# Optimization experiments

Measured on AMD Instinct MI355X. Metric: run time of the kernel, lower is better.

## Reference

```python
import jax, jax.numpy as jnp
import numpy as np

N_EMBD = 1024
N_HEAD = 16
HEAD_DIM = N_EMBD // N_HEAD


def setup_inputs() -> dict:
    key = jax.random.key(0)
    kx, kqkv, kw, kb = jax.random.split(key, 4)
    B, T = 4, 2048
    x = jax.random.normal(kx, (B, T, N_EMBD), dtype=jnp.float32)
    # nn.Linear weights stored [out, in]; apply as x @ W.T
    w_qkv = jax.random.normal(kqkv, (3 * N_EMBD, N_EMBD), dtype=jnp.float32) * (N_EMBD ** -0.5)
    w_out = jax.random.normal(kw, (N_EMBD, N_EMBD), dtype=jnp.float32) * (N_EMBD ** -0.5)
    b_out = jax.random.normal(kb, (N_EMBD,), dtype=jnp.float32) * 0.01
    return {"x": x, "w_qkv": w_qkv, "w_out": w_out, "b_out": b_out}


def reference(x, w_qkv, w_out, b_out):
    B, T, C = x.shape
    H, D = N_HEAD, HEAD_DIM
    qkv = jnp.einsum('btc,fc->btf', x, w_qkv)  # [B,T,3C]
    q, k, v = jnp.split(qkv, 3, axis=-1)
    q = q.reshape(B, T, H, D).transpose(0, 2, 1, 3)  # [B,H,T,D]
    k = k.reshape(B, T, H, D).transpose(0, 2, 1, 3)
    v = v.reshape(B, T, H, D).transpose(0, 2, 1, 3)
    att = jnp.einsum('bhqd,bhkd->bhqk', q, k) * (D ** -0.5)  # [B,H,T,T]
    causal = jnp.tril(jnp.ones((T, T), dtype=bool))
    att = jnp.where(causal[None, None], att, jnp.float32(-jnp.inf))
    att = jax.nn.softmax(att, axis=-1)
    out = jnp.einsum('bhqk,bhkd->bhqd', att, v)  # [B,H,T,D]
    out = out.transpose(0, 2, 1, 3).reshape(B, T, C)
    return jnp.einsum('btc,oc->bto', out, w_out) + b_out
```

## Files before the change

### kernel.cpp

```cpp
#include <hip/hip_runtime.h>
#include <stdint.h>

#define SEQ 2048
#define C3 3072
#define C1 1024

typedef __bf16 bf16x8 __attribute__((ext_vector_type(8)));
typedef short short8 __attribute__((ext_vector_type(8)));
typedef float f32x4 __attribute__((ext_vector_type(4)));
typedef float f32x16 __attribute__((ext_vector_type(16)));
typedef unsigned uintx2 __attribute__((ext_vector_type(2)));
typedef const __attribute__((address_space(1))) void gv_t;
typedef __attribute__((address_space(3))) void lv_t;

#if __has_builtin(__builtin_amdgcn_exp2f)
#define EXP2(x) __builtin_amdgcn_exp2f(x)
#else
#define EXP2(x) exp2f(x)
#endif

static __device__ __forceinline__ unsigned short f2bf(float f) {
  union { float ff; unsigned u; } x; x.ff = f;
  unsigned u = x.u + 0x7FFFu + ((x.u >> 16) & 1u);
  return (unsigned short)(u >> 16);
}
static __device__ __forceinline__ unsigned rne2(float lo, float hi) {
  return (unsigned)f2bf(lo) | ((unsigned)f2bf(hi) << 16);
}
static __device__ __forceinline__ unsigned pk2(float lo, float hi) {
  union { float f; unsigned u; } a, b; a.f = lo; b.f = hi;
  return __builtin_amdgcn_perm(b.u, a.u, 0x07060302);
}

static __device__ __forceinline__ void plswap(unsigned a, unsigned b,
                                              unsigned& o0, unsigned& o1) {
#if __has_builtin(__builtin_amdgcn_permlane32_swap)
  uintx2 r = __builtin_amdgcn_permlane32_swap(a, b, false, false);
  o0 = r[0]; o1 = r[1];
#else
  asm volatile("v_permlane32_swap_b32 %0, %1" : "+v"(a), "+v"(b));
  o0 = a; o1 = b;
#endif
}

__global__ void k_cvt3(const float* __restrict__ ia, const float* __restrict__ ib,
                       const float* __restrict__ ic, unsigned short* __restrict__ oa,
                       unsigned short* __restrict__ ob, unsigned short* __restrict__ oc) {
  int blk = blockIdx.x;
  const float* in; unsigned short* out; int base;
  if (blk < 8192)      { in = ia; out = oa; base = blk; }
  else if (blk < 11264){ in = ib; out = ob; base = blk - 8192; }
  else                 { in = ic; out = oc; base = blk - 11264; }
  int i = base * 256 + threadIdx.x;
  f32x4 v = ((const f32x4*)in)[i];
  ushort4 o;
  o.x = f2bf(v[0]); o.y = f2bf(v[1]); o.z = f2bf(v[2]); o.w = f2bf(v[3]);
  ((ushort4*)out)[i] = o;
}

template<int MODE>
__global__ __launch_bounds__(256, 3) void k_gemm(
    const unsigned short* __restrict__ A, const unsigned short* __restrict__ B,
    void* __restrict__ Cout, const float* __restrict__ bias,
    unsigned short* __restrict__ vTout, int M, int N, int K)
{
  __shared__ unsigned short As[128 * 64];
  __shared__ unsigned short Bs[128 * 64];
  const int tid = threadIdx.x;
  const int w = tid >> 6, l = tid & 63;
  const int lane15 = l & 15, quad = l >> 4;
  const int m0 = blockIdx.y * 128, n0 = blockIdx.x * 128;
  const int wm = (w >> 1) * 64, wn = (w & 1) * 64;

  f32x4 acc[4][4];
#pragma unroll
  for (int i = 0; i < 4; i++)
#pragma unroll
    for (int j = 0; j < 4; j++) acc[i][j] = (f32x4){0.f, 0.f, 0.f, 0.f};

  const int srow = l >> 3;
  const int g_off = ((l & 7) ^ (srow & 7)) * 8;
  const unsigned short* Ab = A + (size_t)(m0 + w * 32 + srow) * K + g_off;
  const unsigned short* Bb = B + (size_t)(n0 + w * 32 + srow) * K + g_off;
  const int rsl = lane15 & 7;

  for (int k0 = 0; k0 < K; k0 += 64) {
    __syncthreads();
#pragma unroll
    for (int i = 0; i < 4; i++) {
      int rb = w * 32 + i * 8;
      __builtin_amdgcn_global_load_lds((gv_t*)(Ab + (size_t)(i * 8) * K + k0),
                                       (lv_t*)&As[rb * 64], 16, 0, 0);
      __builtin_amdgcn_global_load_lds((gv_t*)(Bb + (size_t)(i * 8) * K + k0),
                                       (lv_t*)&Bs[rb * 64], 16, 0, 0);
    }
    __syncthreads();
#pragma unroll
    for (int s = 0; s < 2; s++) {
      bf16x8 af[4], bfr[4];
      const int slot = ((s * 4 + quad) ^ rsl) * 8;
#pragma unroll
      for (int t = 0; t < 4; t++) {
        af[t]  = *(const bf16x8*)&As[(wm + t * 16 + lane15) * 64 + slot];
        bfr[t] = *(const bf16x8*)&Bs[(wn + t * 16 + lane15) * 64 + slot];
      }
#pragma unroll
      for (int i = 0; i < 4; i++)
#pragma unroll
        for (int j = 0; j < 4; j++)
          acc[i][j] = __builtin_amdgcn_mfma_f32_16x16x32_bf16(af[i], bfr[j], acc[i][j], 0, 0, 0);
    }
  }

  if (MODE == 0) {
    if (n0 >= 2048) {
#pragma unroll
      for (int i = 0; i < 4; i++) {
        int rowb = m0 + wm + i * 16 + quad * 4;
        int bb = rowb >> 11, t = rowb & 2047;
#pragma unroll
        for (int j = 0; j < 4; j++) {
          int hd = n0 + wn + j * 16 + lane15 - 2048;
          unsigned short* vp = vTout +
              ((size_t)((bb << 4) + (hd >> 6)) * 64 + (hd & 63)) * SEQ + t;
          *(uint2*)vp = make_uint2(rne2(acc[i][j][0], acc[i][j][1]),
                                   rne2(acc[i][j][2], acc[i][j][3]));
        }
      }
    } else {
      unsigned short* Cp = (unsigned short*)Cout;
      const float s = (n0 < 1024) ? 0.18033688f : 1.0f;
#pragma unroll
      for (int i = 0; i < 4; i++) {
        int rowb = m0 + wm + i * 16 + quad * 4;
#pragma unroll
        for (int j = 0; j < 4; j++) {
          int col = n0 + wn + j * 16 + lane15;
#pragma unroll
          for (int r = 0; r < 4; r++)
            Cp[(size_t)(rowb + r) * N + col] = f2bf(acc[i][j][r] * s);
        }
      }
    }
  } else {
    float* Cp = (float*)Cout;
#pragma unroll
    for (int i = 0; i < 4; i++) {
      int rowb = m0 + wm + i * 16 + quad * 4;
#pragma unroll
      for (int j = 0; j < 4; j++) {
        int col = n0 + wn + j * 16 + lane15;
        float bv = bias[col];
#pragma unroll
        for (int r = 0; r < 4; r++)
          Cp[(size_t)(rowb + r) * N + col] = acc[i][j][r] + bv;
      }
    }
  }
}


static __device__ __forceinline__ void stage_kv(
    unsigned short* bufp, const unsigned short* __restrict__ qkv,
    const unsigned short* __restrict__ vT, size_t tokb, int bh, int h,
    int k0, int w, int krow_l, int kslot, int vrow_l, int vslot)
{
  unsigned short* Kb = bufp;
  unsigned short* Vb = bufp + 8192;
#pragma unroll
  for (int i = 0; i < 4; i++) {
    int rb = (w * 4 + i) * 8;
    int row = rb + krow_l;
    int ck = kslot ^ (row & 7);
    const unsigned short* g = qkv + (tokb + k0 + row) * C3 + C1 + h * 64 + ck * 8;
    __builtin_amdgcn_global_load_lds((gv_t*)g, (lv_t*)&Kb[rb * 64], 16, 0, 0);
  }
#pragma unroll
  for (int i = 0; i < 4; i++) {
    int rb = (w * 4 + i) * 4;
    int row = rb + vrow_l;
    int ck = vslot ^ (row & 15);
    const unsigned short* g = vT + ((size_t)bh * 64 + row) * SEQ + k0 + ck * 8;
    __builtin_amdgcn_global_load_lds((gv_t*)g, (lv_t*)&Vb[rb * 128], 16, 0, 0);
  }
}

static __device__ __forceinline__ void attn_tile(
    f32x16* O, float& lrun, const bf16x8* qf,
    const unsigned short* Kb, const unsigned short* Vb,
    bool diag, int k0, int qmy, int w, int l31, int hl)
{
#pragma unroll
  for (int ht = 0; ht < 2; ht++) {
    if (diag && (ht * 2 > w)) continue;
    const bool two = !diag || (ht * 2 + 1 <= w);

#pragma unroll
    for (int lm = 0; lm < 2; lm++) {
      if (lm == 1 && !two) continue;
      const int mt = ht * 2 + lm;

      f32x16 stL;
#pragma unroll
      for (int i = 0; i < 16; i++) stL[i] = -16.f;
      {
        int row = mt * 32 + l31;
        const unsigned short* kr = &Kb[row * 64];
        __builtin_amdgcn_s_setprio(1);
#pragma unroll
        for (int ks = 0; ks < 4; ks++) {
          bf16x8 a = *(const bf16x8*)&kr[((((ks << 1) | hl)) ^ (row & 7)) * 8];
          stL = __builtin_amdgcn_mfma_f32_32x32x16_bf16(a, qf[ks], stL, 0, 0, 0);
        }
        __builtin_amdgcn_s_setprio(0);
      }

      if (diag && mt == w) {
#pragma unroll
        for (int r = 0; r < 16; r++) {
          int key = k0 + w * 32 + (r & 3) + ((r >> 2) << 3) + (hl << 2);
          if (key > qmy) stL[r] = -1e30f;
        }
      }

      float ps0 = 0.f, ps1 = 0.f, ps2 = 0.f, ps3 = 0.f;
      unsigned pk[8];
#pragma unroll
      for (int r = 0; r < 16; r += 4) {
        float p0 = EXP2(stL[r]);
        float p1 = EXP2(stL[r + 1]);
        float p2 = EXP2(stL[r + 2]);
        float p3 = EXP2(stL[r + 3]);
        ps0 += p0; ps1 += p1; ps2 += p2; ps3 += p3;
        pk[(r >> 1)]     = pk2(p0, p1);
        pk[(r >> 1) + 1] = pk2(p2, p3);
      }
      lrun += (ps0 + ps1) + (ps2 + ps3);

      bf16x8 vf[2][2];
#pragma unroll
      for (int e = 0; e < 2; e++) {
        int kk = ht * 4 + lm * 2 + e;
#pragma unroll
        for (int dt = 0; dt < 2; dt++) {
          int row = dt * 32 + l31;
          vf[e][dt] = *(const bf16x8*)&Vb[row * 128 + (((2 * kk + hl)) ^ (row & 15)) * 8];
        }
      }

#pragma unroll
      for (int e = 0; e < 2; e++) {
        union { unsigned u[4]; bf16x8 v; } Bf;
        plswap(pk[4 * e],     pk[4 * e + 2], Bf.u[0], Bf.u[2]);
        plswap(pk[4 * e + 1], pk[4 * e + 3], Bf.u[1], Bf.u[3]);
        __builtin_amdgcn_s_setprio(1);
        O[0] = __builtin_amdgcn_mfma_f32_32x32x16_bf16(vf[e][0], Bf.v, O[0], 0, 0, 0);
        O[1] = __builtin_amdgcn_mfma_f32_32x32x16_bf16(vf[e][1], Bf.v, O[1], 0, 0, 0);
        __builtin_amdgcn_s_setprio(0);
      }
    }
  }
}

static __device__ __forceinline__ void attn_epi(
    const f32x16* O, float lrun, unsigned short* buf,
    unsigned short* __restrict__ att, size_t tokb, int q0, int h,
    int w, int l, int l31, int hl)
{
  lrun += __shfl_xor(lrun, 32, 64);
  float linv = __builtin_amdgcn_rcpf(lrun);
  unsigned* epi32 = (unsigned*)buf;
  const int base = w * 2304 + l31 * 72;
  __builtin_amdgcn_s_waitcnt(0);
#pragma unroll
  for (int dt = 0; dt < 2; dt++)
#pragma unroll
    for (int c = 0; c < 4; c++) {
      int d0 = dt * 32 + c * 8 + hl * 4;
      epi32[(base + d0) >> 1]     = rne2(O[dt][4 * c] * linv, O[dt][4 * c + 1] * linv);
      epi32[(base + d0 + 2) >> 1] = rne2(O[dt][4 * c + 2] * linv, O[dt][4 * c + 3] * linv);
    }
  __builtin_amdgcn_s_waitcnt(0);
  {
    int q = l >> 1, hf = l & 1;
    const unsigned short* ep = &buf[w * 2304 + q * 72 + hf * 32];
    unsigned short* og = att + (tokb + q0 + w * 32 + q) * C1 + h * 64 + hf * 32;
#pragma unroll
    for (int c2 = 0; c2 < 4; c2++)
      *(bf16x8*)(og + c2 * 8) = *(const bf16x8*)&ep[c2 * 8];
  }
}

__global__ __launch_bounds__(256, 2) void k_attn(
    const unsigned short* __restrict__ qkv, const unsigned short* __restrict__ vT,
    unsigned short* __restrict__ att)
{
  __shared__ unsigned short buf[2][16384];
  const int tid = threadIdx.x;
  const int w = tid >> 6, l = tid & 63;
  const int l31 = l & 31, hl = l >> 5;
  const int bh = blockIdx.x, b = bh >> 4, h = bh & 15;
  const int yq = blockIdx.y;
  const int qt_lo = yq, qt_hi = 15 - yq;
  const int q0l = qt_lo << 7, q0h = qt_hi << 7;
  const int nkt = qt_hi + 1;
  const size_t tokb = (size_t)b * SEQ;
  const int qmy_l = q0l + w * 32 + l31;
  const int qmy_h = q0h + w * 32 + l31;

  const int krow_l = l >> 3, kslot = l & 7;
  const int vrow_l = l >> 4, vslot = l & 15;

  bf16x8 qfh[4], qfl[4];
  {
    const unsigned short* qph = qkv + (tokb + q0h + w * 32 + l31) * C3 + h * 64 + hl * 8;
    const unsigned short* qpl = qkv + (tokb + q0l + w * 32 + l31) * C3 + h * 64 + hl * 8;
#pragma unroll
    for (int ks = 0; ks < 4; ks++) {
      qfh[ks] = *(const bf16x8*)(qph + ks * 16);
      qfl[ks] = *(const bf16x8*)(qpl + ks * 16);
    }
  }

  f32x16 Oh[2], Ol[2];
#pragma unroll
  for (int i = 0; i < 16; i++) { Oh[0][i] = 0.f; Oh[1][i] = 0.f; Ol[0][i] = 0.f; Ol[1][i] = 0.f; }
  float lrh = 0.f, lrl = 0.f;

  stage_kv(&buf[0][0], qkv, vT, tokb, bh, h, 0, w, krow_l, kslot, vrow_l, vslot);

  int cur = 0;
  for (int kt = 0; kt < nkt; kt++) {
    asm volatile("s_waitcnt vmcnt(0)" ::: "memory");
    __builtin_amdgcn_s_barrier();
    if (kt + 1 < nkt)
      stage_kv(&buf[cur ^ 1][0], qkv, vT, tokb, bh, h, (kt + 1) << 7,
               w, krow_l, kslot, vrow_l, vslot);

    const unsigned short* Kb = &buf[cur][0];
    const unsigned short* Vb = &buf[cur][8192];
    const int k0 = kt << 7;

    attn_tile(Oh, lrh, qfh, Kb, Vb, kt == qt_hi, k0, qmy_h, w, l31, hl);
    if (kt <= qt_lo)
      attn_tile(Ol, lrl, qfl, Kb, Vb, kt == qt_lo, k0, qmy_l, w, l31, hl);

    cur ^= 1;
  }

  __syncthreads();
  attn_epi(Oh, lrh, &buf[0][0], att, tokb, q0h, h, w, l, l31, hl);
  attn_epi(Ol, lrl, &buf[0][0], att, tokb, q0l, h, w, l, l31, hl);
}

extern "C" void kernel_launch(void* const* d_in, const int* in_sizes, int n_in,
                              void* d_out, int out_size, void* d_ws, size_t ws_size,
                              hipStream_t stream) {
  const float* x     = (const float*)d_in[0];
  const float* w_qkv = (const float*)d_in[1];
  const float* w_out = (const float*)d_in[2];
  const float* b_out = (const float*)d_in[3];
  float* out = (float*)d_out;

  unsigned short* xb  = (unsigned short*)d_ws;
  unsigned short* wqb = xb  + (size_t)8192 * 1024;
  unsigned short* wob = wqb + (size_t)3072 * 1024;
  unsigned short* qkv = wob + (size_t)1024 * 1024;
  unsigned short* att = qkv + (size_t)8192 * 3072;
  unsigned short* vT  = att + (size_t)8192 * 1024;

  k_cvt3<<<12288, 256, 0, stream>>>(x, w_qkv, w_out, xb, wqb, wob);
  k_gemm<0><<<dim3(24, 64), 256, 0, stream>>>(xb, wqb, (void*)qkv, nullptr, vT, 8192, 3072, 1024);
  k_attn<<<dim3(64, 8), 256, 0, stream>>>(qkv, vT, att);
  k_gemm<1><<<dim3(8, 64), 256, 0, stream>>>(att, wob, (void*)out, b_out, nullptr, 8192, 1024, 1024);
}
```

Before: 221.8 us.

## Read V fragments directly from global memory and stage only K in LDS

```diff
diff --git a/kernel.cpp b/kernel.cpp
--- a/kernel.cpp
+++ b/kernel.cpp
@@ -160,13 +160,10 @@
 }
 
 
-static __device__ __forceinline__ void stage_kv(
-    unsigned short* bufp, const unsigned short* __restrict__ qkv,
-    const unsigned short* __restrict__ vT, size_t tokb, int bh, int h,
-    int k0, int w, int krow_l, int kslot, int vrow_l, int vslot)
-{
-  unsigned short* Kb = bufp;
-  unsigned short* Vb = bufp + 8192;
+static __device__ __forceinline__ void stage_k(
+    unsigned short* Kb, const unsigned short* __restrict__ qkv,
+    size_t tokb, int h, int k0, int w, int krow_l, int kslot)
+{
 #pragma unroll
   for (int i = 0; i < 4; i++) {
     int rb = (w * 4 + i) * 8;
@@ -175,19 +172,11 @@
     const unsigned short* g = qkv + (tokb + k0 + row) * C3 + C1 + h * 64 + ck * 8;
     __builtin_amdgcn_global_load_lds((gv_t*)g, (lv_t*)&Kb[rb * 64], 16, 0, 0);
   }
-#pragma unroll
-  for (int i = 0; i < 4; i++) {
-    int rb = (w * 4 + i) * 4;
-    int row = rb + vrow_l;
-    int ck = vslot ^ (row & 15);
-    const unsigned short* g = vT + ((size_t)bh * 64 + row) * SEQ + k0 + ck * 8;
-    __builtin_amdgcn_global_load_lds((gv_t*)g, (lv_t*)&Vb[rb * 128], 16, 0, 0);
-  }
 }
 
 static __device__ __forceinline__ void attn_tile(
     f32x16* O, float& lrun, const bf16x8* qf,
-    const unsigned short* Kb, const unsigned short* Vb,
+    const unsigned short* Kb, const unsigned short* __restrict__ vTb,
     bool diag, int k0, int qmy, int w, int l31, int hl)
 {
 #pragma unroll
@@ -213,6 +202,17 @@
           stL = __builtin_amdgcn_mfma_f32_32x32x16_bf16(a, qf[ks], stL, 0, 0, 0);
         }
         __builtin_amdgcn_s_setprio(0);
+      }
+
+      bf16x8 vf[2][2];
+#pragma unroll
+      for (int e = 0; e < 2; e++) {
+        int kk = ht * 4 + lm * 2 + e;
+#pragma unroll
+        for (int dt = 0; dt < 2; dt++) {
+          int row = dt * 32 + l31;
+          vf[e][dt] = *(const bf16x8*)&vTb[(size_t)row * SEQ + k0 + (2 * kk + hl) * 8];
+        }
       }
 
       if (diag && mt == w) {
@@ -237,17 +237,6 @@
       }
       lrun += (ps0 + ps1) + (ps2 + ps3);
 
-      bf16x8 vf[2][2];
-#pragma unroll
-      for (int e = 0; e < 2; e++) {
-        int kk = ht * 4 + lm * 2 + e;
-#pragma unroll
-        for (int dt = 0; dt < 2; dt++) {
-          int row = dt * 32 + l31;
-          vf[e][dt] = *(const bf16x8*)&Vb[row * 128 + (((2 * kk + hl)) ^ (row & 15)) * 8];
-        }
-      }
-
 #pragma unroll
       for (int e = 0; e < 2; e++) {
         union { unsigned u[4]; bf16x8 v; } Bf;
@@ -291,11 +280,11 @@
   }
 }
 
-__global__ __launch_bounds__(256, 2) void k_attn(
+__global__ __launch_bounds__(256, 3) void k_attn(
     const unsigned short* __restrict__ qkv, const unsigned short* __restrict__ vT,
     unsigned short* __restrict__ att)
 {
-  __shared__ unsigned short buf[2][16384];
+  __shared__ unsigned short buf[2][8192];
   const int tid = threadIdx.x;
   const int w = tid >> 6, l = tid & 63;
   const int l31 = l & 31, hl = l >> 5;
@@ -309,7 +298,7 @@
   const int qmy_h = q0h + w * 32 + l31;
 
   const int krow_l = l >> 3, kslot = l & 7;
-  const int vrow_l = l >> 4, vslot = l & 15;
+  const unsigned short* vTb = vT + (size_t)bh * 64 * SEQ;
 
   bf16x8 qfh[4], qfl[4];
   {
@@ -327,23 +316,21 @@
   for (int i = 0; i < 16; i++) { Oh[0][i] = 0.f; Oh[1][i] = 0.f; Ol[0][i] = 0.f; Ol[1][i] = 0.f; }
   float lrh = 0.f, lrl = 0.f;
 
-  stage_kv(&buf[0][0], qkv, vT, tokb, bh, h, 0, w, krow_l, kslot, vrow_l, vslot);
+  stage_k(&buf[0][0], qkv, tokb, h, 0, w, krow_l, kslot);
 
   int cur = 0;
   for (int kt = 0; kt < nkt; kt++) {
     asm volatile("s_waitcnt vmcnt(0)" ::: "memory");
     __builtin_amdgcn_s_barrier();
     if (kt + 1 < nkt)
-      stage_kv(&buf[cur ^ 1][0], qkv, vT, tokb, bh, h, (kt + 1) << 7,
-               w, krow_l, kslot, vrow_l, vslot);
+      stage_k(&buf[cur ^ 1][0], qkv, tokb, h, (kt + 1) << 7, w, krow_l, kslot);
 
     const unsigned short* Kb = &buf[cur][0];
-    const unsigned short* Vb = &buf[cur][8192];
     const int k0 = kt << 7;
 
-    attn_tile(Oh, lrh, qfh, Kb, Vb, kt == qt_hi, k0, qmy_h, w, l31, hl);
+    attn_tile(Oh, lrh, qfh, Kb, vTb, kt == qt_hi, k0, qmy_h, w, l31, hl);
     if (kt <= qt_lo)
-      attn_tile(Ol, lrl, qfl, Kb, Vb, kt == qt_lo, k0, qmy_l, w, l31, hl);
+      attn_tile(Ol, lrl, qfl, Kb, vTb, kt == qt_lo, k0, qmy_l, w, l31, hl);
 
     cur ^= 1;
   }
```

New measurement: 287.1 us. 1.29x slower.

## Single-buffer V in attention to fit three blocks per CU; coarsen convert kernel

Applied to the files above, without the earlier changes.

```diff
diff --git a/kernel.cpp b/kernel.cpp
--- a/kernel.cpp
+++ b/kernel.cpp
@@ -48,14 +48,18 @@
                        unsigned short* __restrict__ ob, unsigned short* __restrict__ oc) {
   int blk = blockIdx.x;
   const float* in; unsigned short* out; int base;
-  if (blk < 8192)      { in = ia; out = oa; base = blk; }
-  else if (blk < 11264){ in = ib; out = ob; base = blk - 8192; }
-  else                 { in = ic; out = oc; base = blk - 11264; }
-  int i = base * 256 + threadIdx.x;
-  f32x4 v = ((const f32x4*)in)[i];
-  ushort4 o;
-  o.x = f2bf(v[0]); o.y = f2bf(v[1]); o.z = f2bf(v[2]); o.w = f2bf(v[3]);
-  ((ushort4*)out)[i] = o;
+  if (blk < 2048)     { in = ia; out = oa; base = blk; }
+  else if (blk < 2816){ in = ib; out = ob; base = blk - 2048; }
+  else                { in = ic; out = oc; base = blk - 2816; }
+  int i0 = base * 1024 + threadIdx.x;
+#pragma unroll
+  for (int j = 0; j < 4; j++) {
+    int i = i0 + j * 256;
+    f32x4 v = ((const f32x4*)in)[i];
+    ushort4 o;
+    o.x = f2bf(v[0]); o.y = f2bf(v[1]); o.z = f2bf(v[2]); o.w = f2bf(v[3]);
+    ((ushort4*)out)[i] = o;
+  }
 }
 
 template<int MODE>
@@ -160,13 +164,10 @@
 }
 
 
-static __device__ __forceinline__ void stage_kv(
-    unsigned short* bufp, const unsigned short* __restrict__ qkv,
-    const unsigned short* __restrict__ vT, size_t tokb, int bh, int h,
-    int k0, int w, int krow_l, int kslot, int vrow_l, int vslot)
-{
-  unsigned short* Kb = bufp;
-  unsigned short* Vb = bufp + 8192;
+static __device__ __forceinline__ void stage_k(
+    unsigned short* Kb, const unsigned short* __restrict__ qkv,
+    size_t tokb, int h, int k0, int w, int krow_l, int kslot)
+{
 #pragma unroll
   for (int i = 0; i < 4; i++) {
     int rb = (w * 4 + i) * 8;
@@ -175,6 +176,12 @@
     const unsigned short* g = qkv + (tokb + k0 + row) * C3 + C1 + h * 64 + ck * 8;
     __builtin_amdgcn_global_load_lds((gv_t*)g, (lv_t*)&Kb[rb * 64], 16, 0, 0);
   }
+}
+
+static __device__ __forceinline__ void stage_v(
+    unsigned short* Vb, const unsigned short* __restrict__ vT,
+    int bh, int k0, int w, int vrow_l, int vslot)
+{
 #pragma unroll
   for (int i = 0; i < 4; i++) {
     int rb = (w * 4 + i) * 4;
@@ -291,11 +298,12 @@
   }
 }
 
-__global__ __launch_bounds__(256, 2) void k_attn(
+__global__ __launch_bounds__(256, 3) void k_attn(
     const unsigned short* __restrict__ qkv, const unsigned short* __restrict__ vT,
     unsigned short* __restrict__ att)
 {
-  __shared__ unsigned short buf[2][16384];
+  __shared__ unsigned short bufK[2][8192];
+  __shared__ unsigned short bufV[8192];
   const int tid = threadIdx.x;
   const int w = tid >> 6, l = tid & 63;
   const int l31 = l & 31, hl = l >> 5;
@@ -327,30 +335,33 @@
   for (int i = 0; i < 16; i++) { Oh[0][i] = 0.f; Oh[1][i] = 0.f; Ol[0][i] = 0.f; Ol[1][i] = 0.f; }
   float lrh = 0.f, lrl = 0.f;
 
-  stage_kv(&buf[0][0], qkv, vT, tokb, bh, h, 0, w, krow_l, kslot, vrow_l, vslot);
+  stage_k(&bufK[0][0], qkv, tokb, h, 0, w, krow_l, kslot);
+  stage_v(&bufV[0], vT, bh, 0, w, vrow_l, vslot);
 
   int cur = 0;
   for (int kt = 0; kt < nkt; kt++) {
     asm volatile("s_waitcnt vmcnt(0)" ::: "memory");
     __builtin_amdgcn_s_barrier();
     if (kt + 1 < nkt)
-      stage_kv(&buf[cur ^ 1][0], qkv, vT, tokb, bh, h, (kt + 1) << 7,
-               w, krow_l, kslot, vrow_l, vslot);
-
-    const unsigned short* Kb = &buf[cur][0];
-    const unsigned short* Vb = &buf[cur][8192];
+      stage_k(&bufK[cur ^ 1][0], qkv, tokb, h, (kt + 1) << 7, w, krow_l, kslot);
+
+    const unsigned short* Kb = &bufK[cur][0];
     const int k0 = kt << 7;
 
-    attn_tile(Oh, lrh, qfh, Kb, Vb, kt == qt_hi, k0, qmy_h, w, l31, hl);
+    attn_tile(Oh, lrh, qfh, Kb, bufV, kt == qt_hi, k0, qmy_h, w, l31, hl);
     if (kt <= qt_lo)
-      attn_tile(Ol, lrl, qfl, Kb, Vb, kt == qt_lo, k0, qmy_l, w, l31, hl);
+      attn_tile(Ol, lrl, qfl, Kb, bufV, kt == qt_lo, k0, qmy_l, w, l31, hl);
+
+    __builtin_amdgcn_s_barrier();
+    if (kt + 1 < nkt)
+      stage_v(&bufV[0], vT, bh, (kt + 1) << 7, w, vrow_l, vslot);
 
     cur ^= 1;
   }
 
   __syncthreads();
-  attn_epi(Oh, lrh, &buf[0][0], att, tokb, q0h, h, w, l, l31, hl);
-  attn_epi(Ol, lrl, &buf[0][0], att, tokb, q0l, h, w, l, l31, hl);
+  attn_epi(Oh, lrh, &bufK[0][0], att, tokb, q0h, h, w, l, l31, hl);
+  attn_epi(Ol, lrl, &bufK[0][0], att, tokb, q0l, h, w, l, l31, hl);
 }
 
 extern "C" void kernel_launch(void* const* d_in, const int* in_sizes, int n_in,
@@ -369,7 +380,7 @@
   unsigned short* att = qkv + (size_t)8192 * 3072;
   unsigned short* vT  = att + (size_t)8192 * 1024;
 
-  k_cvt3<<<12288, 256, 0, stream>>>(x, w_qkv, w_out, xb, wqb, wob);
+  k_cvt3<<<3072, 256, 0, stream>>>(x, w_qkv, w_out, xb, wqb, wob);
   k_gemm<0><<<dim3(24, 64), 256, 0, stream>>>(xb, wqb, (void*)qkv, nullptr, vT, 8192, 3072, 1024);
   k_attn<<<dim3(64, 8), 256, 0, stream>>>(qkv, vT, att);
   k_gemm<1><<<dim3(8, 64), 256, 0, stream>>>(att, wob, (void*)out, b_out, nullptr, 8192, 1024, 1024);
```

Result: slower. 257.5 us (+16.1%).

## Split hi/lo query tiles across eight waves in attention; widen cast kernel work

Applied to the files above, without the earlier changes.

```diff
diff --git a/kernel.cpp b/kernel.cpp
--- a/kernel.cpp
+++ b/kernel.cpp
@@ -48,14 +48,18 @@
                        unsigned short* __restrict__ ob, unsigned short* __restrict__ oc) {
   int blk = blockIdx.x;
   const float* in; unsigned short* out; int base;
-  if (blk < 8192)      { in = ia; out = oa; base = blk; }
-  else if (blk < 11264){ in = ib; out = ob; base = blk - 8192; }
-  else                 { in = ic; out = oc; base = blk - 11264; }
-  int i = base * 256 + threadIdx.x;
-  f32x4 v = ((const f32x4*)in)[i];
-  ushort4 o;
-  o.x = f2bf(v[0]); o.y = f2bf(v[1]); o.z = f2bf(v[2]); o.w = f2bf(v[3]);
-  ((ushort4*)out)[i] = o;
+  if (blk < 2048)     { in = ia; out = oa; base = blk; }
+  else if (blk < 2816){ in = ib; out = ob; base = blk - 2048; }
+  else                { in = ic; out = oc; base = blk - 2816; }
+  int i0 = base * 1024 + threadIdx.x;
+#pragma unroll
+  for (int j = 0; j < 4; j++) {
+    int i = i0 + j * 256;
+    f32x4 v = ((const f32x4*)in)[i];
+    ushort4 o;
+    o.x = f2bf(v[0]); o.y = f2bf(v[1]); o.z = f2bf(v[2]); o.w = f2bf(v[3]);
+    ((ushort4*)out)[i] = o;
+  }
 }
 
 template<int MODE>
@@ -163,21 +167,23 @@
 static __device__ __forceinline__ void stage_kv(
     unsigned short* bufp, const unsigned short* __restrict__ qkv,
     const unsigned short* __restrict__ vT, size_t tokb, int bh, int h,
-    int k0, int w, int krow_l, int kslot, int vrow_l, int vslot)
+    int k0, int w, int l)
 {
   unsigned short* Kb = bufp;
   unsigned short* Vb = bufp + 8192;
-#pragma unroll
-  for (int i = 0; i < 4; i++) {
-    int rb = (w * 4 + i) * 8;
+  const int krow_l = l >> 3, kslot = l & 7;
+  const int vrow_l = l >> 4, vslot = l & 15;
+#pragma unroll
+  for (int i = 0; i < 2; i++) {
+    int rb = (w * 2 + i) * 8;
     int row = rb + krow_l;
     int ck = kslot ^ (row & 7);
     const unsigned short* g = qkv + (tokb + k0 + row) * C3 + C1 + h * 64 + ck * 8;
     __builtin_amdgcn_global_load_lds((gv_t*)g, (lv_t*)&Kb[rb * 64], 16, 0, 0);
   }
 #pragma unroll
-  for (int i = 0; i < 4; i++) {
-    int rb = (w * 4 + i) * 4;
+  for (int i = 0; i < 2; i++) {
+    int rb = (w * 2 + i) * 4;
     int row = rb + vrow_l;
     int ck = vslot ^ (row & 15);
     const unsigned short* g = vT + ((size_t)bh * 64 + row) * SEQ + k0 + ck * 8;
@@ -188,12 +194,12 @@
 static __device__ __forceinline__ void attn_tile(
     f32x16* O, float& lrun, const bf16x8* qf,
     const unsigned short* Kb, const unsigned short* Vb,
-    bool diag, int k0, int qmy, int w, int l31, int hl)
+    bool diag, int k0, int qmy, int w4, int l31, int hl)
 {
 #pragma unroll
   for (int ht = 0; ht < 2; ht++) {
-    if (diag && (ht * 2 > w)) continue;
-    const bool two = !diag || (ht * 2 + 1 <= w);
+    if (diag && (ht * 2 > w4)) continue;
+    const bool two = !diag || (ht * 2 + 1 <= w4);
 
 #pragma unroll
     for (int lm = 0; lm < 2; lm++) {
@@ -215,10 +221,10 @@
         __builtin_amdgcn_s_setprio(0);
       }
 
-      if (diag && mt == w) {
+      if (diag && mt == w4) {
 #pragma unroll
         for (int r = 0; r < 16; r++) {
-          int key = k0 + w * 32 + (r & 3) + ((r >> 2) << 3) + (hl << 2);
+          int key = k0 + w4 * 32 + (r & 3) + ((r >> 2) << 3) + (hl << 2);
           if (key > qmy) stL[r] = -1e30f;
         }
       }
@@ -264,14 +270,13 @@
 
 static __device__ __forceinline__ void attn_epi(
     const f32x16* O, float lrun, unsigned short* buf,
-    unsigned short* __restrict__ att, size_t tokb, int q0, int h,
+    unsigned short* __restrict__ att, size_t tokb, int qwbase, int h,
     int w, int l, int l31, int hl)
 {
   lrun += __shfl_xor(lrun, 32, 64);
   float linv = __builtin_amdgcn_rcpf(lrun);
   unsigned* epi32 = (unsigned*)buf;
   const int base = w * 2304 + l31 * 72;
-  __builtin_amdgcn_s_waitcnt(0);
 #pragma unroll
   for (int dt = 0; dt < 2; dt++)
 #pragma unroll
@@ -284,73 +289,63 @@
   {
     int q = l >> 1, hf = l & 1;
     const unsigned short* ep = &buf[w * 2304 + q * 72 + hf * 32];
-    unsigned short* og = att + (tokb + q0 + w * 32 + q) * C1 + h * 64 + hf * 32;
+    unsigned short* og = att + (tokb + qwbase + q) * C1 + h * 64 + hf * 32;
 #pragma unroll
     for (int c2 = 0; c2 < 4; c2++)
       *(bf16x8*)(og + c2 * 8) = *(const bf16x8*)&ep[c2 * 8];
   }
 }
 
-__global__ __launch_bounds__(256, 2) void k_attn(
+__global__ __launch_bounds__(512, 2) void k_attn(
     const unsigned short* __restrict__ qkv, const unsigned short* __restrict__ vT,
     unsigned short* __restrict__ att)
 {
   __shared__ unsigned short buf[2][16384];
   const int tid = threadIdx.x;
   const int w = tid >> 6, l = tid & 63;
+  const int w4 = w & 3;
+  const bool hi = (w < 4);
   const int l31 = l & 31, hl = l >> 5;
   const int bh = blockIdx.x, b = bh >> 4, h = bh & 15;
   const int yq = blockIdx.y;
   const int qt_lo = yq, qt_hi = 15 - yq;
-  const int q0l = qt_lo << 7, q0h = qt_hi << 7;
+  const int myqt = hi ? qt_hi : qt_lo;
+  const int q0 = myqt << 7;
   const int nkt = qt_hi + 1;
   const size_t tokb = (size_t)b * SEQ;
-  const int qmy_l = q0l + w * 32 + l31;
-  const int qmy_h = q0h + w * 32 + l31;
-
-  const int krow_l = l >> 3, kslot = l & 7;
-  const int vrow_l = l >> 4, vslot = l & 15;
-
-  bf16x8 qfh[4], qfl[4];
+  const int qw = q0 + w4 * 32;
+  const int qmy = qw + l31;
+
+  bf16x8 qf[4];
   {
-    const unsigned short* qph = qkv + (tokb + q0h + w * 32 + l31) * C3 + h * 64 + hl * 8;
-    const unsigned short* qpl = qkv + (tokb + q0l + w * 32 + l31) * C3 + h * 64 + hl * 8;
-#pragma unroll
-    for (int ks = 0; ks < 4; ks++) {
-      qfh[ks] = *(const bf16x8*)(qph + ks * 16);
-      qfl[ks] = *(const bf16x8*)(qpl + ks * 16);
-    }
-  }
-
-  f32x16 Oh[2], Ol[2];
-#pragma unroll
-  for (int i = 0; i < 16; i++) { Oh[0][i] = 0.f; Oh[1][i] = 0.f; Ol[0][i] = 0.f; Ol[1][i] = 0.f; }
-  float lrh = 0.f, lrl = 0.f;
-
-  stage_kv(&buf[0][0], qkv, vT, tokb, bh, h, 0, w, krow_l, kslot, vrow_l, vslot);
+    const unsigned short* qp = qkv + (tokb + qw + l31) * C3 + h * 64 + hl * 8;
+#pragma unroll
+    for (int ks = 0; ks < 4; ks++) qf[ks] = *(const bf16x8*)(qp + ks * 16);
+  }
+
+  f32x16 O[2];
+#pragma unroll
+  for (int i = 0; i < 16; i++) { O[0][i] = 0.f; O[1][i] = 0.f; }
+  float lrun = 0.f;
+
+  stage_kv(&buf[0][0], qkv, vT, tokb, bh, h, 0, w, l);
 
   int cur = 0;
   for (int kt = 0; kt < nkt; kt++) {
     asm volatile("s_waitcnt vmcnt(0)" ::: "memory");
     __builtin_amdgcn_s_barrier();
     if (kt + 1 < nkt)
-      stage_kv(&buf[cur ^ 1][0], qkv, vT, tokb, bh, h, (kt + 1) << 7,
-               w, krow_l, kslot, vrow_l, vslot);
-
-    const unsigned short* Kb = &buf[cur][0];
-    const unsigned short* Vb = &buf[cur][8192];
-    const int k0 = kt << 7;
-
-    attn_tile(Oh, lrh, qfh, Kb, Vb, kt == qt_hi, k0, qmy_h, w, l31, hl);
-    if (kt <= qt_lo)
-      attn_tile(Ol, lrl, qfl, Kb, Vb, kt == qt_lo, k0, qmy_l, w, l31, hl);
+      stage_kv(&buf[cur ^ 1][0], qkv, vT, tokb, bh, h, (kt + 1) << 7, w, l);
+
+    if (kt <= myqt)
+      attn_tile(O, lrun, qf, &buf[cur][0], &buf[cur][8192],
+                kt == myqt, kt << 7, qmy, w4, l31, hl);
 
     cur ^= 1;
   }
 
   __syncthreads();
-  attn_epi(Oh, lrh, &buf[0][0], att, tokb, q0h, h, w, l, l31, hl);
-  attn_epi(Ol, lrl, &buf[0][0], att, tokb, q0l, h, w, l, l31, hl);
+  attn_epi(O, lrun, &buf[0][0], att, tokb, qw, h, w, l, l31, hl);
 }
 
 extern "C" void kernel_launch(void* const* d_in, const int* in_sizes, int n_in,
@@ -369,8 +364,8 @@
   unsigned short* att = qkv + (size_t)8192 * 3072;
   unsigned short* vT  = att + (size_t)8192 * 1024;
 
-  k_cvt3<<<12288, 256, 0, stream>>>(x, w_qkv, w_out, xb, wqb, wob);
+  k_cvt3<<<3072, 256, 0, stream>>>(x, w_qkv, w_out, xb, wqb, wob);
   k_gemm<0><<<dim3(24, 64), 256, 0, stream>>>(xb, wqb, (void*)qkv, nullptr, vT, 8192, 3072, 1024);
-  k_attn<<<dim3(64, 8), 256, 0, stream>>>(qkv, vT, att);
+  k_attn<<<dim3(64, 8), 512, 0, stream>>>(qkv, vT, att);
   k_gemm<1><<<dim3(8, 64), 256, 0, stream>>>(att, wob, (void*)out, b_out, nullptr, 8192, 1024, 1024);
 }
```

Result: slower. 229.5 us (+3.5%).
